# Performance work log

Measured on AMD Instinct MI355X. Metric: run time of the kernel, lower is better.

Reference implementation:

```python
import jax, jax.numpy as jnp
import numpy as np

N = 20480      # total nodes
E = 327680     # total edges (avg degree 16)
B = 16         # graphs in batch
IN = 16        # node feature dim
H = 8          # hidden_out_channel
CO = 64        # conv_out_channel
ET = 36        # n_edge_types
EF = 2         # edge_features
OUT = 1        # classifier out
DIMS = [(IN, H), (H, H), (H, H), (H, CO)]


def setup_inputs() -> dict:
    key = jax.random.key(0)
    ks = jax.random.split(key, 32)
    inp = {}
    inp['x'] = jax.random.normal(ks[0], (N, IN), jnp.float32)
    inp['edge_index'] = jax.random.randint(ks[1], (2, E), 0, N)
    inp['edge_type'] = jax.random.randint(ks[2], (E,), 0, ET)
    inp['edge_attr'] = jax.random.normal(ks[3], (E, EF), jnp.float32)
    inp['cell_type'] = jax.random.randint(ks[4], (N,), 0, 2)
    inp['batch'] = (jnp.arange(N) // (N // B)).astype(jnp.int32)
    i = 5
    for l, (ci, co) in enumerate(DIMS, 1):
        d = ci * co
        s = 1.0 / np.sqrt(EF)
        inp[f'emb{l}'] = jax.random.normal(ks[i], (ET, d), jnp.float32) * 0.02; i += 1
        inp[f'wh{l}'] = jax.random.normal(ks[i], (EF, d), jnp.float32) * s; i += 1
        inp[f'bh{l}'] = jnp.zeros((d,), jnp.float32)
        inp[f'wg{l}'] = jax.random.normal(ks[i], (EF, d), jnp.float32) * s; i += 1
        inp[f'bg{l}'] = jnp.zeros((d,), jnp.float32)
        inp[f'root{l}'] = jax.random.normal(ks[i], (ci, co), jnp.float32) / np.sqrt(ci); i += 1
        inp[f'bias{l}'] = jnp.zeros((co,), jnp.float32)
    inp['clf_w'] = jax.random.normal(ks[i], (CO, OUT), jnp.float32) / np.sqrt(CO)
    inp['clf_b'] = jnp.zeros((OUT,), jnp.float32)
    return inp


def edge_weights(etype, ef, emb, wh, bh, wg, bg):
    # EdgeNN: relu(embedding(type) * fc_h(feat) + fc_g(feat)) -> [E, cin*cout]
    return jax.nn.relu(emb[etype] * (ef @ wh + bh) + (ef @ wg + bg))


def nnconv(h, src, dst, W, root, bias):
    # NNConv(aggr='mean', root_weight=True): gather src feats, per-edge matmul, scatter-mean
    cin, cout = root.shape
    msg = jnp.einsum('ei,eio->eo', h[src], W.reshape(-1, cin, cout))  # [E, cout]
    agg = jax.ops.segment_sum(msg, dst, num_segments=N)
    deg = jax.ops.segment_sum(jnp.ones_like(msg[:, 0]), dst, num_segments=N)
    return agg / jnp.maximum(deg, 1.0)[:, None] + h @ root + bias


def reference(x, edge_index, edge_type, edge_attr, cell_type, batch,
              emb1, wh1, bh1, wg1, bg1, root1, bias1,
              emb2, wh2, bh2, wg2, bg2, root2, bias2,
              emb3, wh3, bh3, wg3, bg3, root3, bias3,
              emb4, wh4, bh4, wg4, bg4, root4, bias4,
              clf_w, clf_b):
    src, dst = edge_index[0], edge_index[1]
    layers = [(emb1, wh1, bh1, wg1, bg1, root1, bias1),
              (emb2, wh2, bh2, wg2, bg2, root2, bias2),
              (emb3, wh3, bh3, wg3, bg3, root3, bias3),
              (emb4, wh4, bh4, wg4, bg4, root4, bias4)]
    h = x
    for (emb, wh, bh, wg, bg, root, bias) in layers:  # fixed 4 structurally-distinct layers
        W = edge_weights(edge_type, edge_attr, emb, wh, bh, wg, bg)
        h = jax.nn.relu(nnconv(h, src, dst, W, root, bias))
    # gated scatter-mean pooling over tumor cells (cell_type == 1)
    gate = (cell_type == 1).astype(jnp.int32)
    seg = gate * (batch.astype(jnp.int32) + 1)  # 0 = masked-out bucket
    pooled = jax.ops.segment_sum(h, seg, num_segments=B + 1)
    cnt = jax.ops.segment_sum(jnp.ones((h.shape[0],), h.dtype), seg, num_segments=B + 1)
    pooled = (pooled / jnp.maximum(cnt, 1.0)[:, None])[1:B + 1]  # [B, CO]
    return jax.nn.sigmoid(pooled @ clf_w + clf_b)  # hazards [B, OUT]
```

## Files before the change

kernel.cpp:

```cpp
#include <hip/hip_runtime.h>
#include <math.h>

#define NN 20480
#define NE 327680
#define NBATCH 16

typedef float v2f __attribute__((ext_vector_type(2)));

#if __has_builtin(__builtin_elementwise_max)
#define VMAX0(a) __builtin_elementwise_max((a), (v2f){0.f, 0.f})
#else
static __device__ __forceinline__ v2f VMAX0(v2f a) {
  v2f r; r.x = fmaxf(a.x, 0.f); r.y = fmaxf(a.y, 0.f); return r;
}
#endif

__global__ void hist_kernel(const int* __restrict__ dst, int* __restrict__ cnt) {
  int e = blockIdx.x * blockDim.x + threadIdx.x;
  if (e < NE) atomicAdd(&cnt[dst[e]], 1);
}

__global__ __launch_bounds__(1024) void scan_kernel(const int* __restrict__ cnt,
                                                    int* __restrict__ off,
                                                    int* __restrict__ cur) {
  __shared__ int part[1024];
  int tid = threadIdx.x;
  const int PT = NN / 1024;
  int loc[PT];
  int run = 0;
  int base = tid * PT;
#pragma unroll
  for (int k = 0; k < PT; k++) { loc[k] = run; run += cnt[base + k]; }
  part[tid] = run;
  __syncthreads();
  for (int d = 1; d < 1024; d <<= 1) {
    int t = (tid >= d) ? part[tid - d] : 0;
    __syncthreads();
    part[tid] += t;
    __syncthreads();
  }
  int pre = (tid == 0) ? 0 : part[tid - 1];
#pragma unroll
  for (int k = 0; k < PT; k++) {
    off[base + k] = pre + loc[k];
    cur[base + k] = pre + loc[k];
  }
  if (tid == 1023) off[NN] = pre + run;
}

__global__ void scatter_kernel(const int* __restrict__ src, const int* __restrict__ dst,
                               const int* __restrict__ etype, const float* __restrict__ eattr,
                               int* __restrict__ cur, float4* __restrict__ es) {
  int e = blockIdx.x * blockDim.x + threadIdx.x;
  if (e >= NE) return;
  int d = dst[e];
  int pos = atomicAdd(&cur[d], 1);
  es[pos] = make_float4(__int_as_float(src[e]), __int_as_float(etype[e]),
                        eattr[2 * e], eattr[2 * e + 1]);
}

__global__ __launch_bounds__(256) void transpose_kernel(
    const float* __restrict__ e1, const float* __restrict__ e2,
    const float* __restrict__ e3, const float* __restrict__ e4,
    float* __restrict__ t1, float* __restrict__ t2,
    float* __restrict__ t3, float* __restrict__ t4) {
  int idx = blockIdx.x * 256 + threadIdx.x;
  if (idx < 36 * 128) {
    int t = idx >> 7, r = idx & 127, o = r >> 4, i = r & 15;
    t1[idx] = e1[(t << 7) + i * 8 + o];
  }
  if (idx < 36 * 64) {
    int t = idx >> 6, r = idx & 63, o = r >> 3, i = r & 7;
    t2[idx] = e2[(t << 6) + i * 8 + o];
    t3[idx] = e3[(t << 6) + i * 8 + o];
  }
  {
    int t = idx >> 9, r = idx & 511, o = r >> 3, i = r & 7;
    t4[idx] = e4[(t << 9) + i * 64 + o];
  }
}

__global__ __launch_bounds__(256) void layer_small16(
    const int* __restrict__ off, const float4* __restrict__ es,
    const float* __restrict__ h_in, const float* __restrict__ embT,
    const float* __restrict__ wh, const float* __restrict__ bh,
    const float* __restrict__ wg, const float* __restrict__ bg,
    const float* __restrict__ root, const float* __restrict__ bias,
    float* __restrict__ h_out) {
  constexpr int D = 128;
  int lane = threadIdx.x & 63;
  int o = lane & 7;
  int ihalf = (lane >> 3) & 1;
  int esub = lane >> 4;
  int ibase = ihalf * 8;
  v2f rwh0[4], rwh1[4], rbh[4], rwg0[4], rwg1[4], rbg[4], rroot[4];
#pragma unroll
  for (int p = 0; p < 4; p++) {
    int a = (ibase + 2 * p) * 8 + o, b = (ibase + 2 * p + 1) * 8 + o;
    rwh0[p] = (v2f){wh[a], wh[b]};
    rwh1[p] = (v2f){wh[D + a], wh[D + b]};
    rbh[p]  = (v2f){bh[a], bh[b]};
    rwg0[p] = (v2f){wg[a], wg[b]};
    rwg1[p] = (v2f){wg[D + a], wg[D + b]};
    rbg[p]  = (v2f){bg[a], bg[b]};
    rroot[p] = (v2f){root[a], root[b]};
  }
  float rbias = bias[o];
  int n = __builtin_amdgcn_readfirstlane((int)(blockIdx.x * 4) + (int)(threadIdx.x >> 6));
  int beg = off[n], end = off[n + 1];
  int nIter = (end - beg + 3) >> 2;
  float acc = 0.f;
  int j = beg + esub;
  bool val0 = j < end;
  float4 rec0 = val0 ? es[j] : make_float4(0.f, 0.f, 0.f, 0.f);
  int s0 = __float_as_int(rec0.x);
  const float4* hp0 = (const float4*)(h_in + s0 * 16 + ibase);
  float4 hA0 = hp0[0], hB0 = hp0[1];
  for (int it = 0; it < nIter; ++it) {
    int j1 = j + 4;
    bool val1 = j1 < end;
    float4 rec1 = val1 ? es[j1] : make_float4(0.f, 0.f, 0.f, 0.f);
    int s1 = __float_as_int(rec1.x);
    const float4* hp1 = (const float4*)(h_in + s1 * 16 + ibase);
    float4 hA1 = hp1[0], hB1 = hp1[1];
    int t0 = __float_as_int(rec0.y);
    const float4* sp = (const float4*)(embT + t0 * 128 + o * 16 + ibase);
    float4 sv0 = sp[0], sv1 = sp[1];
    v2f stv[4] = {(v2f){sv0.x, sv0.y}, (v2f){sv0.z, sv0.w},
                  (v2f){sv1.x, sv1.y}, (v2f){sv1.z, sv1.w}};
    v2f hv[4] = {(v2f){hA0.x, hA0.y}, (v2f){hA0.z, hA0.w},
                 (v2f){hB0.x, hB0.y}, (v2f){hB0.z, hB0.w}};
    v2f ef0 = (v2f){rec0.z, rec0.z}, ef1 = (v2f){rec0.w, rec0.w};
    v2f msg = {0.f, 0.f};
#pragma unroll
    for (int p = 0; p < 4; p++) {
      v2f hval = ef0 * rwh0[p] + ef1 * rwh1[p] + rbh[p];
      v2f gval = ef0 * rwg0[p] + ef1 * rwg1[p] + rbg[p];
      msg += hv[p] * VMAX0(stv[p] * hval + gval);
    }
    acc += val0 ? (msg.x + msg.y) : 0.f;
    rec0 = rec1; hA0 = hA1; hB0 = hB1; val0 = val1; j = j1;
  }
  acc += __shfl_xor(acc, 8);
  acc += __shfl_xor(acc, 16);
  acc += __shfl_xor(acc, 32);
  const float* hn = h_in + n * 16 + ibase;
  v2f rtv = {0.f, 0.f};
#pragma unroll
  for (int p = 0; p < 4; p++)
    rtv += (v2f){hn[2 * p], hn[2 * p + 1]} * rroot[p];
  float rt = rtv.x + rtv.y;
  rt += __shfl_xor(rt, 8);
  float deg = (float)(end - beg);
  float val = fmaxf(rbias + rt + acc / fmaxf(deg, 1.f), 0.f);
  if (lane < 8) h_out[n * 8 + o] = val;
}

__global__ __launch_bounds__(256) void layer_small8(
    const int* __restrict__ off, const float4* __restrict__ es,
    const float* __restrict__ h_in, const float* __restrict__ embT,
    const float* __restrict__ wh, const float* __restrict__ bh,
    const float* __restrict__ wg, const float* __restrict__ bg,
    const float* __restrict__ root, const float* __restrict__ bias,
    float* __restrict__ h_out) {
  int lane = threadIdx.x & 63;
  int o = lane & 7, esub = lane >> 3;
  v2f rwh0[4], rwh1[4], rbh[4], rwg0[4], rwg1[4], rbg[4], rroot[4];
#pragma unroll
  for (int p = 0; p < 4; p++) {
    int a = (2 * p) * 8 + o, b = (2 * p + 1) * 8 + o;
    rwh0[p] = (v2f){wh[a], wh[b]};
    rwh1[p] = (v2f){wh[64 + a], wh[64 + b]};
    rbh[p]  = (v2f){bh[a], bh[b]};
    rwg0[p] = (v2f){wg[a], wg[b]};
    rwg1[p] = (v2f){wg[64 + a], wg[64 + b]};
    rbg[p]  = (v2f){bg[a], bg[b]};
    rroot[p] = (v2f){root[a], root[b]};
  }
  float rbias = bias[o];
  int n = __builtin_amdgcn_readfirstlane((int)(blockIdx.x * 4) + (int)(threadIdx.x >> 6));
  int beg = off[n], end = off[n + 1];
  int nIter = (end - beg + 7) >> 3;
  float acc = 0.f;
  int j = beg + esub;
  bool val0 = j < end;
  float4 rec0 = val0 ? es[j] : make_float4(0.f, 0.f, 0.f, 0.f);
  int s0 = __float_as_int(rec0.x);
  const float4* hp0 = (const float4*)(h_in + s0 * 8);
  float4 hA0 = hp0[0], hB0 = hp0[1];
  for (int it = 0; it < nIter; ++it) {
    int j1 = j + 8;
    bool val1 = j1 < end;
    float4 rec1 = val1 ? es[j1] : make_float4(0.f, 0.f, 0.f, 0.f);
    int s1 = __float_as_int(rec1.x);
    const float4* hp1 = (const float4*)(h_in + s1 * 8);
    float4 hA1 = hp1[0], hB1 = hp1[1];
    int t0 = __float_as_int(rec0.y);
    const float4* sp = (const float4*)(embT + t0 * 64 + o * 8);
    float4 sv0 = sp[0], sv1 = sp[1];
    v2f stv[4] = {(v2f){sv0.x, sv0.y}, (v2f){sv0.z, sv0.w},
                  (v2f){sv1.x, sv1.y}, (v2f){sv1.z, sv1.w}};
    v2f hv[4] = {(v2f){hA0.x, hA0.y}, (v2f){hA0.z, hA0.w},
                 (v2f){hB0.x, hB0.y}, (v2f){hB0.z, hB0.w}};
    v2f ef0 = (v2f){rec0.z, rec0.z}, ef1 = (v2f){rec0.w, rec0.w};
    v2f msg = {0.f, 0.f};
#pragma unroll
    for (int p = 0; p < 4; p++) {
      v2f hval = ef0 * rwh0[p] + ef1 * rwh1[p] + rbh[p];
      v2f gval = ef0 * rwg0[p] + ef1 * rwg1[p] + rbg[p];
      msg += hv[p] * VMAX0(stv[p] * hval + gval);
    }
    acc += val0 ? (msg.x + msg.y) : 0.f;
    rec0 = rec1; hA0 = hA1; hB0 = hB1; val0 = val1; j = j1;
  }
  acc += __shfl_xor(acc, 8);
  acc += __shfl_xor(acc, 16);
  acc += __shfl_xor(acc, 32);
  const float* hn = h_in + n * 8;
  v2f rtv = {0.f, 0.f};
#pragma unroll
  for (int p = 0; p < 4; p++)
    rtv += (v2f){hn[2 * p], hn[2 * p + 1]} * rroot[p];
  float deg = (float)(end - beg);
  float val = fmaxf(rbias + rtv.x + rtv.y + acc / fmaxf(deg, 1.f), 0.f);
  if (lane < 8) h_out[n * 8 + o] = val;
}

__global__ __launch_bounds__(256) void layer_l4(
    const int* __restrict__ off, const float4* __restrict__ es,
    const float* __restrict__ h_in, const float* __restrict__ embT,
    const float* __restrict__ wh, const float* __restrict__ bh,
    const float* __restrict__ wg, const float* __restrict__ bg,
    const float* __restrict__ root, const float* __restrict__ bias,
    float* __restrict__ h_out) {
  int lane = threadIdx.x & 63;
  v2f rwh0[4], rwh1[4], rbh[4], rwg0[4], rwg1[4], rbg[4], rroot[4];
#pragma unroll
  for (int p = 0; p < 4; p++) {
    int a = (2 * p) * 64 + lane, b = (2 * p + 1) * 64 + lane;
    rwh0[p] = (v2f){wh[a], wh[b]};
    rwh1[p] = (v2f){wh[512 + a], wh[512 + b]};
    rbh[p]  = (v2f){bh[a], bh[b]};
    rwg0[p] = (v2f){wg[a], wg[b]};
    rwg1[p] = (v2f){wg[512 + a], wg[512 + b]};
    rbg[p]  = (v2f){bg[a], bg[b]};
    rroot[p] = (v2f){root[a], root[b]};
  }
  float rbias = bias[lane];
  int n = __builtin_amdgcn_readfirstlane((int)(blockIdx.x * 4) + (int)(threadIdx.x >> 6));
  int beg = off[n], end = off[n + 1];
  float acc0 = 0.f, acc1 = 0.f;
  int e = beg;
  for (; e + 2 <= end; e += 2) {
    float4 r0 = es[e], r1 = es[e + 1];
    int s0 = __float_as_int(r0.x), t0 = __float_as_int(r0.y);
    int s1 = __float_as_int(r1.x), t1 = __float_as_int(r1.y);
    const float4* hp0 = (const float4*)(h_in + s0 * 8);
    const float4* hp1 = (const float4*)(h_in + s1 * 8);
    float4 a0 = hp0[0], a1 = hp0[1];
    float4 b0 = hp1[0], b1 = hp1[1];
    const float4* ep0 = (const float4*)(embT + t0 * 512 + lane * 8);
    const float4* ep1 = (const float4*)(embT + t1 * 512 + lane * 8);
    float4 s00 = ep0[0], s01 = ep0[1];
    float4 s10 = ep1[0], s11 = ep1[1];
    v2f sv0[4] = {(v2f){s00.x, s00.y}, (v2f){s00.z, s00.w},
                  (v2f){s01.x, s01.y}, (v2f){s01.z, s01.w}};
    v2f sv1[4] = {(v2f){s10.x, s10.y}, (v2f){s10.z, s10.w},
                  (v2f){s11.x, s11.y}, (v2f){s11.z, s11.w}};
    v2f hva[4] = {(v2f){a0.x, a0.y}, (v2f){a0.z, a0.w},
                  (v2f){a1.x, a1.y}, (v2f){a1.z, a1.w}};
    v2f hvb[4] = {(v2f){b0.x, b0.y}, (v2f){b0.z, b0.w},
                  (v2f){b1.x, b1.y}, (v2f){b1.z, b1.w}};
    v2f e00 = (v2f){r0.z, r0.z}, e01 = (v2f){r0.w, r0.w};
    v2f e10 = (v2f){r1.z, r1.z}, e11 = (v2f){r1.w, r1.w};
    v2f m0 = {0.f, 0.f}, m1 = {0.f, 0.f};
#pragma unroll
    for (int p = 0; p < 4; p++) {
      v2f hv0 = e00 * rwh0[p] + e01 * rwh1[p] + rbh[p];
      v2f gv0 = e00 * rwg0[p] + e01 * rwg1[p] + rbg[p];
      m0 += hva[p] * VMAX0(sv0[p] * hv0 + gv0);
      v2f hv1 = e10 * rwh0[p] + e11 * rwh1[p] + rbh[p];
      v2f gv1 = e10 * rwg0[p] + e11 * rwg1[p] + rbg[p];
      m1 += hvb[p] * VMAX0(sv1[p] * hv1 + gv1);
    }
    acc0 += m0.x + m0.y;
    acc1 += m1.x + m1.y;
  }
  if (e < end) {
    float4 r0 = es[e];
    int s0 = __float_as_int(r0.x), t0 = __float_as_int(r0.y);
    const float4* hp0 = (const float4*)(h_in + s0 * 8);
    float4 a0 = hp0[0], a1 = hp0[1];
    const float4* ep0 = (const float4*)(embT + t0 * 512 + lane * 8);
    float4 s00 = ep0[0], s01 = ep0[1];
    v2f sv0[4] = {(v2f){s00.x, s00.y}, (v2f){s00.z, s00.w},
                  (v2f){s01.x, s01.y}, (v2f){s01.z, s01.w}};
    v2f hva[4] = {(v2f){a0.x, a0.y}, (v2f){a0.z, a0.w},
                  (v2f){a1.x, a1.y}, (v2f){a1.z, a1.w}};
    v2f e00 = (v2f){r0.z, r0.z}, e01 = (v2f){r0.w, r0.w};
    v2f m0 = {0.f, 0.f};
#pragma unroll
    for (int p = 0; p < 4; p++) {
      v2f hv0 = e00 * rwh0[p] + e01 * rwh1[p] + rbh[p];
      v2f gv0 = e00 * rwg0[p] + e01 * rwg1[p] + rbg[p];
      m0 += hva[p] * VMAX0(sv0[p] * hv0 + gv0);
    }
    acc0 += m0.x + m0.y;
  }
  float acc = acc0 + acc1;
  float deg = (float)(end - beg);
  const float* hn = h_in + n * 8;
  v2f rtv = {0.f, 0.f};
#pragma unroll
  for (int p = 0; p < 4; p++)
    rtv += (v2f){hn[2 * p], hn[2 * p + 1]} * rroot[p];
  h_out[n * 64 + lane] = fmaxf(rbias + rtv.x + rtv.y + acc / fmaxf(deg, 1.f), 0.f);
}

__global__ __launch_bounds__(256) void pool1_kernel(
    const float* __restrict__ h4, const int* __restrict__ ct,
    float* __restrict__ pooled, float* __restrict__ pcnt) {
  __shared__ float ss[4][64];
  __shared__ float sc[4];
  int b = blockIdx.x / 20, c = blockIdx.x % 20;
  int base = b * (NN / NBATCH) + c * 64;
  int o = threadIdx.x & 63, sub = threadIdx.x >> 6;
  float sum = 0.f, cnt = 0.f;
  for (int j = sub; j < 64; j += 4) {
    int n = base + j;
    if (ct[n] == 1) { sum += h4[n * 64 + o]; cnt += 1.f; }
  }
  ss[sub][o] = sum;
  if (o == 0) sc[sub] = cnt;
  __syncthreads();
  if (threadIdx.x < 64) {
    float tot = ss[0][o] + ss[1][o] + ss[2][o] + ss[3][o];
    unsafeAtomicAdd(&pooled[b * 64 + o], tot);
    if (o == 0) unsafeAtomicAdd(&pcnt[b], sc[0] + sc[1] + sc[2] + sc[3]);
  }
}

__global__ __launch_bounds__(1024) void pool2_kernel(
    const float* __restrict__ pooled, const float* __restrict__ pcnt,
    const float* __restrict__ clf_w, const float* __restrict__ clf_b,
    float* __restrict__ out) {
  int b = threadIdx.x >> 6, o = threadIdx.x & 63;
  float c = pcnt[b];
  float v = (pooled[b * 64 + o] / fmaxf(c, 1.f)) * clf_w[o];
#pragma unroll
  for (int d = 32; d; d >>= 1) v += __shfl_down(v, d);
  if (o == 0) out[b] = 1.f / (1.f + expf(-(v + clf_b[0])));
}

extern "C" void kernel_launch(void* const* d_in, const int* in_sizes, int n_in,
                              void* d_out, int out_size, void* d_ws, size_t ws_size,
                              hipStream_t stream) {
  (void)in_sizes; (void)n_in; (void)out_size; (void)ws_size;
  const float* x     = (const float*)d_in[0];
  const int*   eidx  = (const int*)d_in[1];
  const int*   src   = eidx;
  const int*   dst   = eidx + NE;
  const int*   etype = (const int*)d_in[2];
  const float* eattr = (const float*)d_in[3];
  const int*   ct    = (const int*)d_in[4];
  const float *emb[4], *wh[4], *bh[4], *wg[4], *bg[4], *root[4], *bias[4];
  for (int l = 0; l < 4; l++) {
    int b0 = 6 + 7 * l;
    emb[l]  = (const float*)d_in[b0 + 0];
    wh[l]   = (const float*)d_in[b0 + 1];
    bh[l]   = (const float*)d_in[b0 + 2];
    wg[l]   = (const float*)d_in[b0 + 3];
    bg[l]   = (const float*)d_in[b0 + 4];
    root[l] = (const float*)d_in[b0 + 5];
    bias[l] = (const float*)d_in[b0 + 6];
  }
  const float* clf_w = (const float*)d_in[34];
  const float* clf_b = (const float*)d_in[35];
  float* outp = (float*)d_out;

  float* ws  = (float*)d_ws;
  int*    off    = (int*)ws;
  float4* es     = (float4*)(ws + 20484);
  float*  hA     = ws + 20484 + 4 * NE;
  float*  hB     = hA + 8 * NN;
  float*  h4     = hB + 8 * NN;
  float*  embT1  = h4 + 64 * NN;
  float*  embT2  = embT1 + 36 * 128;
  float*  embT3  = embT2 + 36 * 64;
  float*  embT4  = embT3 + 36 * 64;
  float*  pooled = embT4 + 36 * 512;
  float*  pcnt   = pooled + 16 * 64;
  int*    cnt    = (int*)h4;
  int*    cur    = cnt + NN;

  hipMemsetAsync(cnt, 0, NN * sizeof(int), stream);
  hipMemsetAsync(pooled, 0, (16 * 64 + 16) * sizeof(float), stream);
  hist_kernel<<<NE / 256, 256, 0, stream>>>(dst, cnt);
  transpose_kernel<<<72, 256, 0, stream>>>(emb[0], emb[1], emb[2], emb[3],
                                           embT1, embT2, embT3, embT4);
  scan_kernel<<<1, 1024, 0, stream>>>(cnt, off, cur);
  scatter_kernel<<<NE / 256, 256, 0, stream>>>(src, dst, etype, eattr, cur, es);

  layer_small16<<<NN / 4, 256, 0, stream>>>(off, es, x, embT1,
      wh[0], bh[0], wg[0], bg[0], root[0], bias[0], hA);
  layer_small8<<<NN / 4, 256, 0, stream>>>(off, es, hA, embT2,
      wh[1], bh[1], wg[1], bg[1], root[1], bias[1], hB);
  layer_small8<<<NN / 4, 256, 0, stream>>>(off, es, hB, embT3,
      wh[2], bh[2], wg[2], bg[2], root[2], bias[2], hA);
  layer_l4<<<NN / 4, 256, 0, stream>>>(off, es, hA, embT4,
      wh[3], bh[3], wg[3], bg[3], root[3], bias[3], h4);

  pool1_kernel<<<320, 256, 0, stream>>>(h4, ct, pooled, pcnt);
  pool2_kernel<<<1, 1024, 0, stream>>>(pooled, pcnt, clf_w, clf_b, outp);
}
```

Baseline: 305.4 us.

## Fuse all stages into one persistent kernel with software grid barriers

Replaces the chain of separate launches (histogram, scan, scatter, four layers, pooling) with one persistent kernel of 240 blocks of 1024 threads. The stages are separated by an atomic-counter grid barrier. The scan becomes a two-level block scan, and the layer loops become grid-stride loops over nodes, one wave per node, using a ballot-driven edge loop. This removes launch gaps and memsets, but adds barrier latency, depends on all 240 blocks being co-resident, and may lower occupancy.

```diff
diff --git a/kernel.cpp b/kernel.cpp
--- a/kernel.cpp
+++ b/kernel.cpp
@@ -4,159 +4,118 @@
 #define NN 20480
 #define NE 327680
 #define NBATCH 16
+#define NBLK 240
+#define NTHR 1024
+#define GSZ (NBLK * NTHR)
+#define NWAVE (NBLK * (NTHR / 64))
+#define NPB ((NN + NBLK - 1) / NBLK)
 
 typedef float v2f __attribute__((ext_vector_type(2)));
 
-#if __has_builtin(__builtin_elementwise_max)
-#define VMAX0(a) __builtin_elementwise_max((a), (v2f){0.f, 0.f})
-#else
-static __device__ __forceinline__ v2f VMAX0(v2f a) {
+static __device__ __forceinline__ v2f vmax0(v2f a) {
   v2f r; r.x = fmaxf(a.x, 0.f); r.y = fmaxf(a.y, 0.f); return r;
 }
-#endif
-
-__global__ void hist_kernel(const int* __restrict__ dst, int* __restrict__ cnt) {
-  int e = blockIdx.x * blockDim.x + threadIdx.x;
-  if (e < NE) atomicAdd(&cnt[dst[e]], 1);
-}
-
-__global__ __launch_bounds__(1024) void scan_kernel(const int* __restrict__ cnt,
-                                                    int* __restrict__ off,
-                                                    int* __restrict__ cur) {
-  __shared__ int part[1024];
-  int tid = threadIdx.x;
-  const int PT = NN / 1024;
-  int loc[PT];
-  int run = 0;
-  int base = tid * PT;
-#pragma unroll
-  for (int k = 0; k < PT; k++) { loc[k] = run; run += cnt[base + k]; }
-  part[tid] = run;
+
+struct Args {
+  const float* x; const int* src; const int* dst; const int* etype;
+  const float* eattr; const int* ct;
+  const float* emb[4]; const float* wh[4]; const float* bh[4];
+  const float* wg[4]; const float* bg[4]; const float* root[4]; const float* bias[4];
+  const float* clf_w; const float* clf_b;
+  float* out;
+  int* off; float4* es; float* hA; float* hB; float* h4;
+  float* eT1; float* eT2; float* eT3; float* eT4;
+  float* pooled; float* pcnt; int* cnt; int* cur; int* bar; int* partial;
+};
+
+__device__ __forceinline__ void grid_sync(int* cntp, int* genp) {
   __syncthreads();
-  for (int d = 1; d < 1024; d <<= 1) {
-    int t = (tid >= d) ? part[tid - d] : 0;
-    __syncthreads();
-    part[tid] += t;
-    __syncthreads();
-  }
-  int pre = (tid == 0) ? 0 : part[tid - 1];
-#pragma unroll
-  for (int k = 0; k < PT; k++) {
-    off[base + k] = pre + loc[k];
-    cur[base + k] = pre + loc[k];
-  }
-  if (tid == 1023) off[NN] = pre + run;
-}
-
-__global__ void scatter_kernel(const int* __restrict__ src, const int* __restrict__ dst,
-                               const int* __restrict__ etype, const float* __restrict__ eattr,
-                               int* __restrict__ cur, float4* __restrict__ es) {
-  int e = blockIdx.x * blockDim.x + threadIdx.x;
-  if (e >= NE) return;
-  int d = dst[e];
-  int pos = atomicAdd(&cur[d], 1);
-  es[pos] = make_float4(__int_as_float(src[e]), __int_as_float(etype[e]),
-                        eattr[2 * e], eattr[2 * e + 1]);
-}
-
-__global__ __launch_bounds__(256) void transpose_kernel(
-    const float* __restrict__ e1, const float* __restrict__ e2,
-    const float* __restrict__ e3, const float* __restrict__ e4,
-    float* __restrict__ t1, float* __restrict__ t2,
-    float* __restrict__ t3, float* __restrict__ t4) {
-  int idx = blockIdx.x * 256 + threadIdx.x;
-  if (idx < 36 * 128) {
-    int t = idx >> 7, r = idx & 127, o = r >> 4, i = r & 15;
-    t1[idx] = e1[(t << 7) + i * 8 + o];
-  }
-  if (idx < 36 * 64) {
-    int t = idx >> 6, r = idx & 63, o = r >> 3, i = r & 7;
-    t2[idx] = e2[(t << 6) + i * 8 + o];
-    t3[idx] = e3[(t << 6) + i * 8 + o];
-  }
-  {
-    int t = idx >> 9, r = idx & 511, o = r >> 3, i = r & 7;
-    t4[idx] = e4[(t << 9) + i * 64 + o];
-  }
-}
-
-__global__ __launch_bounds__(256) void layer_small16(
-    const int* __restrict__ off, const float4* __restrict__ es,
-    const float* __restrict__ h_in, const float* __restrict__ embT,
-    const float* __restrict__ wh, const float* __restrict__ bh,
-    const float* __restrict__ wg, const float* __restrict__ bg,
-    const float* __restrict__ root, const float* __restrict__ bias,
-    float* __restrict__ h_out) {
-  constexpr int D = 128;
+  if (threadIdx.x == 0) {
+    __threadfence();
+    int g = __hip_atomic_load(genp, __ATOMIC_RELAXED, __HIP_MEMORY_SCOPE_AGENT);
+    int c = __hip_atomic_fetch_add(cntp, 1, __ATOMIC_ACQ_REL, __HIP_MEMORY_SCOPE_AGENT);
+    if (c == NBLK - 1) {
+      __hip_atomic_store(cntp, 0, __ATOMIC_RELAXED, __HIP_MEMORY_SCOPE_AGENT);
+      __hip_atomic_store(genp, g + 1, __ATOMIC_RELEASE, __HIP_MEMORY_SCOPE_AGENT);
+    } else {
+      while (__hip_atomic_load(genp, __ATOMIC_ACQUIRE, __HIP_MEMORY_SCOPE_AGENT) == g)
+        __builtin_amdgcn_s_sleep(4);
+    }
+    __threadfence();
+  }
+  __syncthreads();
+}
+
+__device__ __forceinline__ void do_small16(const Args& a) {
+  const int D = 128;
   int lane = threadIdx.x & 63;
-  int o = lane & 7;
-  int ihalf = (lane >> 3) & 1;
-  int esub = lane >> 4;
+  int o = lane & 7, ihalf = (lane >> 3) & 1, esub = lane >> 4;
   int ibase = ihalf * 8;
+  const float *wh = a.wh[0], *bh = a.bh[0], *wg = a.wg[0], *bg = a.bg[0];
+  const float *root = a.root[0], *bias = a.bias[0];
   v2f rwh0[4], rwh1[4], rbh[4], rwg0[4], rwg1[4], rbg[4], rroot[4];
 #pragma unroll
   for (int p = 0; p < 4; p++) {
-    int a = (ibase + 2 * p) * 8 + o, b = (ibase + 2 * p + 1) * 8 + o;
-    rwh0[p] = (v2f){wh[a], wh[b]};
-    rwh1[p] = (v2f){wh[D + a], wh[D + b]};
-    rbh[p]  = (v2f){bh[a], bh[b]};
-    rwg0[p] = (v2f){wg[a], wg[b]};
-    rwg1[p] = (v2f){wg[D + a], wg[D + b]};
-    rbg[p]  = (v2f){bg[a], bg[b]};
-    rroot[p] = (v2f){root[a], root[b]};
+    int ai = (ibase + 2 * p) * 8 + o, bi = (ibase + 2 * p + 1) * 8 + o;
+    rwh0[p] = (v2f){wh[ai], wh[bi]};  rwh1[p] = (v2f){wh[D + ai], wh[D + bi]};
+    rbh[p]  = (v2f){bh[ai], bh[bi]};
+    rwg0[p] = (v2f){wg[ai], wg[bi]};  rwg1[p] = (v2f){wg[D + ai], wg[D + bi]};
+    rbg[p]  = (v2f){bg[ai], bg[bi]};  rroot[p] = (v2f){root[ai], root[bi]};
   }
   float rbias = bias[o];
-  int n = __builtin_amdgcn_readfirstlane((int)(blockIdx.x * 4) + (int)(threadIdx.x >> 6));
-  int beg = off[n], end = off[n + 1];
-  int nIter = (end - beg + 3) >> 2;
-  float acc = 0.f;
-  int j = beg + esub;
-  bool val0 = j < end;
-  float4 rec0 = val0 ? es[j] : make_float4(0.f, 0.f, 0.f, 0.f);
-  int s0 = __float_as_int(rec0.x);
-  const float4* hp0 = (const float4*)(h_in + s0 * 16 + ibase);
-  float4 hA0 = hp0[0], hB0 = hp0[1];
-  for (int it = 0; it < nIter; ++it) {
-    int j1 = j + 4;
-    bool val1 = j1 < end;
-    float4 rec1 = val1 ? es[j1] : make_float4(0.f, 0.f, 0.f, 0.f);
-    int s1 = __float_as_int(rec1.x);
-    const float4* hp1 = (const float4*)(h_in + s1 * 16 + ibase);
-    float4 hA1 = hp1[0], hB1 = hp1[1];
-    int t0 = __float_as_int(rec0.y);
-    const float4* sp = (const float4*)(embT + t0 * 128 + o * 16 + ibase);
-    float4 sv0 = sp[0], sv1 = sp[1];
-    v2f stv[4] = {(v2f){sv0.x, sv0.y}, (v2f){sv0.z, sv0.w},
-                  (v2f){sv1.x, sv1.y}, (v2f){sv1.z, sv1.w}};
-    v2f hv[4] = {(v2f){hA0.x, hA0.y}, (v2f){hA0.z, hA0.w},
-                 (v2f){hB0.x, hB0.y}, (v2f){hB0.z, hB0.w}};
-    v2f ef0 = (v2f){rec0.z, rec0.z}, ef1 = (v2f){rec0.w, rec0.w};
-    v2f msg = {0.f, 0.f};
-#pragma unroll
-    for (int p = 0; p < 4; p++) {
-      v2f hval = ef0 * rwh0[p] + ef1 * rwh1[p] + rbh[p];
-      v2f gval = ef0 * rwg0[p] + ef1 * rwg1[p] + rbg[p];
-      msg += hv[p] * VMAX0(stv[p] * hval + gval);
-    }
-    acc += val0 ? (msg.x + msg.y) : 0.f;
-    rec0 = rec1; hA0 = hA1; hB0 = hB1; val0 = val1; j = j1;
-  }
-  acc += __shfl_xor(acc, 8);
-  acc += __shfl_xor(acc, 16);
-  acc += __shfl_xor(acc, 32);
-  const float* hn = h_in + n * 16 + ibase;
-  v2f rtv = {0.f, 0.f};
-#pragma unroll
-  for (int p = 0; p < 4; p++)
-    rtv += (v2f){hn[2 * p], hn[2 * p + 1]} * rroot[p];
-  float rt = rtv.x + rtv.y;
-  rt += __shfl_xor(rt, 8);
-  float deg = (float)(end - beg);
-  float val = fmaxf(rbias + rt + acc / fmaxf(deg, 1.f), 0.f);
-  if (lane < 8) h_out[n * 8 + o] = val;
-}
-
-__global__ __launch_bounds__(256) void layer_small8(
+  int wid = blockIdx.x * (NTHR / 64) + (threadIdx.x >> 6);
+  for (int n0 = wid; n0 < NN; n0 += NWAVE) {
+    int n = __builtin_amdgcn_readfirstlane(n0);
+    int beg = a.off[n], end = a.off[n + 1];
+    float acc = 0.f;
+    int j = beg + esub;
+    bool v0 = j < end;
+    float4 rec0 = v0 ? a.es[j] : make_float4(0.f, 0.f, 0.f, 0.f);
+    int s0 = __float_as_int(rec0.x);
+    const float4* hp0 = (const float4*)(a.x + s0 * 16 + ibase);
+    float4 hA0 = hp0[0], hB0 = hp0[1];
+    while (__ballot(v0)) {
+      int j1 = j + 4;
+      bool v1 = j1 < end;
+      float4 rec1 = v1 ? a.es[j1] : make_float4(0.f, 0.f, 0.f, 0.f);
+      int s1 = __float_as_int(rec1.x);
+      const float4* hp1 = (const float4*)(a.x + s1 * 16 + ibase);
+      float4 hA1 = hp1[0], hB1 = hp1[1];
+      int t0 = __float_as_int(rec0.y);
+      const float4* sp = (const float4*)(a.eT1 + t0 * 128 + o * 16 + ibase);
+      float4 sv0 = sp[0], sv1 = sp[1];
+      v2f stv[4] = {(v2f){sv0.x, sv0.y}, (v2f){sv0.z, sv0.w},
+                    (v2f){sv1.x, sv1.y}, (v2f){sv1.z, sv1.w}};
+      v2f hv[4] = {(v2f){hA0.x, hA0.y}, (v2f){hA0.z, hA0.w},
+                   (v2f){hB0.x, hB0.y}, (v2f){hB0.z, hB0.w}};
+      v2f ef0 = (v2f){rec0.z, rec0.z}, ef1 = (v2f){rec0.w, rec0.w};
+      v2f msg = {0.f, 0.f};
+#pragma unroll
+      for (int p = 0; p < 4; p++) {
+        v2f hval = ef0 * rwh0[p] + ef1 * rwh1[p] + rbh[p];
+        v2f gval = ef0 * rwg0[p] + ef1 * rwg1[p] + rbg[p];
+        msg += hv[p] * vmax0(stv[p] * hval + gval);
+      }
+      acc += v0 ? (msg.x + msg.y) : 0.f;
+      rec0 = rec1; hA0 = hA1; hB0 = hB1; v0 = v1; j = j1;
+    }
+    acc += __shfl_xor(acc, 8);
+    acc += __shfl_xor(acc, 16);
+    acc += __shfl_xor(acc, 32);
+    const float* hn = a.x + n * 16 + ibase;
+    v2f rtv = {0.f, 0.f};
+#pragma unroll
+    for (int p = 0; p < 4; p++)
+      rtv += (v2f){hn[2 * p], hn[2 * p + 1]} * rroot[p];
+    float rt = rtv.x + rtv.y;
+    rt += __shfl_xor(rt, 8);
+    float deg = (float)(end - beg);
+    float val = fmaxf(rbias + rt + acc / fmaxf(deg, 1.f), 0.f);
+    if (lane < 8) a.hA[n * 8 + o] = val;
+  }
+}
+
+__device__ __forceinline__ void do_small8(
     const int* __restrict__ off, const float4* __restrict__ es,
     const float* __restrict__ h_in, const float* __restrict__ embT,
     const float* __restrict__ wh, const float* __restrict__ bh,
@@ -168,248 +127,323 @@
   v2f rwh0[4], rwh1[4], rbh[4], rwg0[4], rwg1[4], rbg[4], rroot[4];
 #pragma unroll
   for (int p = 0; p < 4; p++) {
-    int a = (2 * p) * 8 + o, b = (2 * p + 1) * 8 + o;
-    rwh0[p] = (v2f){wh[a], wh[b]};
-    rwh1[p] = (v2f){wh[64 + a], wh[64 + b]};
-    rbh[p]  = (v2f){bh[a], bh[b]};
-    rwg0[p] = (v2f){wg[a], wg[b]};
-    rwg1[p] = (v2f){wg[64 + a], wg[64 + b]};
-    rbg[p]  = (v2f){bg[a], bg[b]};
-    rroot[p] = (v2f){root[a], root[b]};
+    int ai = (2 * p) * 8 + o, bi = (2 * p + 1) * 8 + o;
+    rwh0[p] = (v2f){wh[ai], wh[bi]};  rwh1[p] = (v2f){wh[64 + ai], wh[64 + bi]};
+    rbh[p]  = (v2f){bh[ai], bh[bi]};
+    rwg0[p] = (v2f){wg[ai], wg[bi]};  rwg1[p] = (v2f){wg[64 + ai], wg[64 + bi]};
+    rbg[p]  = (v2f){bg[ai], bg[bi]};  rroot[p] = (v2f){root[ai], root[bi]};
   }
   float rbias = bias[o];
-  int n = __builtin_amdgcn_readfirstlane((int)(blockIdx.x * 4) + (int)(threadIdx.x >> 6));
-  int beg = off[n], end = off[n + 1];
-  int nIter = (end - beg + 7) >> 3;
-  float acc = 0.f;
-  int j = beg + esub;
-  bool val0 = j < end;
-  float4 rec0 = val0 ? es[j] : make_float4(0.f, 0.f, 0.f, 0.f);
-  int s0 = __float_as_int(rec0.x);
-  const float4* hp0 = (const float4*)(h_in + s0 * 8);
-  float4 hA0 = hp0[0], hB0 = hp0[1];
-  for (int it = 0; it < nIter; ++it) {
-    int j1 = j + 8;
-    bool val1 = j1 < end;
-    float4 rec1 = val1 ? es[j1] : make_float4(0.f, 0.f, 0.f, 0.f);
-    int s1 = __float_as_int(rec1.x);
-    const float4* hp1 = (const float4*)(h_in + s1 * 8);
-    float4 hA1 = hp1[0], hB1 = hp1[1];
-    int t0 = __float_as_int(rec0.y);
-    const float4* sp = (const float4*)(embT + t0 * 64 + o * 8);
-    float4 sv0 = sp[0], sv1 = sp[1];
-    v2f stv[4] = {(v2f){sv0.x, sv0.y}, (v2f){sv0.z, sv0.w},
-                  (v2f){sv1.x, sv1.y}, (v2f){sv1.z, sv1.w}};
-    v2f hv[4] = {(v2f){hA0.x, hA0.y}, (v2f){hA0.z, hA0.w},
-                 (v2f){hB0.x, hB0.y}, (v2f){hB0.z, hB0.w}};
-    v2f ef0 = (v2f){rec0.z, rec0.z}, ef1 = (v2f){rec0.w, rec0.w};
-    v2f msg = {0.f, 0.f};
-#pragma unroll
-    for (int p = 0; p < 4; p++) {
-      v2f hval = ef0 * rwh0[p] + ef1 * rwh1[p] + rbh[p];
-      v2f gval = ef0 * rwg0[p] + ef1 * rwg1[p] + rbg[p];
-      msg += hv[p] * VMAX0(stv[p] * hval + gval);
-    }
-    acc += val0 ? (msg.x + msg.y) : 0.f;
-    rec0 = rec1; hA0 = hA1; hB0 = hB1; val0 = val1; j = j1;
-  }
-  acc += __shfl_xor(acc, 8);
-  acc += __shfl_xor(acc, 16);
-  acc += __shfl_xor(acc, 32);
-  const float* hn = h_in + n * 8;
-  v2f rtv = {0.f, 0.f};
-#pragma unroll
-  for (int p = 0; p < 4; p++)
-    rtv += (v2f){hn[2 * p], hn[2 * p + 1]} * rroot[p];
-  float deg = (float)(end - beg);
-  float val = fmaxf(rbias + rtv.x + rtv.y + acc / fmaxf(deg, 1.f), 0.f);
-  if (lane < 8) h_out[n * 8 + o] = val;
-}
-
-__global__ __launch_bounds__(256) void layer_l4(
-    const int* __restrict__ off, const float4* __restrict__ es,
-    const float* __restrict__ h_in, const float* __restrict__ embT,
-    const float* __restrict__ wh, const float* __restrict__ bh,
-    const float* __restrict__ wg, const float* __restrict__ bg,
-    const float* __restrict__ root, const float* __restrict__ bias,
-    float* __restrict__ h_out) {
+  int wid = blockIdx.x * (NTHR / 64) + (threadIdx.x >> 6);
+  for (int n0 = wid; n0 < NN; n0 += NWAVE) {
+    int n = __builtin_amdgcn_readfirstlane(n0);
+    int beg = off[n], end = off[n + 1];
+    float acc = 0.f;
+    int j = beg + esub;
+    bool v0 = j < end;
+    float4 rec0 = v0 ? es[j] : make_float4(0.f, 0.f, 0.f, 0.f);
+    int s0 = __float_as_int(rec0.x);
+    const float4* hp0 = (const float4*)(h_in + s0 * 8);
+    float4 hA0 = hp0[0], hB0 = hp0[1];
+    while (__ballot(v0)) {
+      int j1 = j + 8;
+      bool v1 = j1 < end;
+      float4 rec1 = v1 ? es[j1] : make_float4(0.f, 0.f, 0.f, 0.f);
+      int s1 = __float_as_int(rec1.x);
+      const float4* hp1 = (const float4*)(h_in + s1 * 8);
+      float4 hA1 = hp1[0], hB1 = hp1[1];
+      int t0 = __float_as_int(rec0.y);
+      const float4* sp = (const float4*)(embT + t0 * 64 + o * 8);
+      float4 sv0 = sp[0], sv1 = sp[1];
+      v2f stv[4] = {(v2f){sv0.x, sv0.y}, (v2f){sv0.z, sv0.w},
+                    (v2f){sv1.x, sv1.y}, (v2f){sv1.z, sv1.w}};
+      v2f hv[4] = {(v2f){hA0.x, hA0.y}, (v2f){hA0.z, hA0.w},
+                   (v2f){hB0.x, hB0.y}, (v2f){hB0.z, hB0.w}};
+      v2f ef0 = (v2f){rec0.z, rec0.z}, ef1 = (v2f){rec0.w, rec0.w};
+      v2f msg = {0.f, 0.f};
+#pragma unroll
+      for (int p = 0; p < 4; p++) {
+        v2f hval = ef0 * rwh0[p] + ef1 * rwh1[p] + rbh[p];
+        v2f gval = ef0 * rwg0[p] + ef1 * rwg1[p] + rbg[p];
+        msg += hv[p] * vmax0(stv[p] * hval + gval);
+      }
+      acc += v0 ? (msg.x + msg.y) : 0.f;
+      rec0 = rec1; hA0 = hA1; hB0 = hB1; v0 = v1; j = j1;
+    }
+    acc += __shfl_xor(acc, 8);
+    acc += __shfl_xor(acc, 16);
+    acc += __shfl_xor(acc, 32);
+    const float* hn = h_in + n * 8;
+    v2f rtv = {0.f, 0.f};
+#pragma unroll
+    for (int p = 0; p < 4; p++)
+      rtv += (v2f){hn[2 * p], hn[2 * p + 1]} * rroot[p];
+    float deg = (float)(end - beg);
+    float val = fmaxf(rbias + rtv.x + rtv.y + acc / fmaxf(deg, 1.f), 0.f);
+    if (lane < 8) h_out[n * 8 + o] = val;
+  }
+}
+
+__device__ __forceinline__ void do_l4(const Args& a) {
   int lane = threadIdx.x & 63;
+  const float *wh = a.wh[3], *bh = a.bh[3], *wg = a.wg[3], *bg = a.bg[3];
+  const float *root = a.root[3], *bias = a.bias[3];
+  const float* embT = a.eT4;
+  const float* h_in = a.hA;
   v2f rwh0[4], rwh1[4], rbh[4], rwg0[4], rwg1[4], rbg[4], rroot[4];
 #pragma unroll
   for (int p = 0; p < 4; p++) {
-    int a = (2 * p) * 64 + lane, b = (2 * p + 1) * 64 + lane;
-    rwh0[p] = (v2f){wh[a], wh[b]};
-    rwh1[p] = (v2f){wh[512 + a], wh[512 + b]};
-    rbh[p]  = (v2f){bh[a], bh[b]};
-    rwg0[p] = (v2f){wg[a], wg[b]};
-    rwg1[p] = (v2f){wg[512 + a], wg[512 + b]};
-    rbg[p]  = (v2f){bg[a], bg[b]};
-    rroot[p] = (v2f){root[a], root[b]};
+    int ai = (2 * p) * 64 + lane, bi = (2 * p + 1) * 64 + lane;
+    rwh0[p] = (v2f){wh[ai], wh[bi]};  rwh1[p] = (v2f){wh[512 + ai], wh[512 + bi]};
+    rbh[p]  = (v2f){bh[ai], bh[bi]};
+    rwg0[p] = (v2f){wg[ai], wg[bi]};  rwg1[p] = (v2f){wg[512 + ai], wg[512 + bi]};
+    rbg[p]  = (v2f){bg[ai], bg[bi]};  rroot[p] = (v2f){root[ai], root[bi]};
   }
   float rbias = bias[lane];
-  int n = __builtin_amdgcn_readfirstlane((int)(blockIdx.x * 4) + (int)(threadIdx.x >> 6));
-  int beg = off[n], end = off[n + 1];
-  float acc0 = 0.f, acc1 = 0.f;
-  int e = beg;
-  for (; e + 2 <= end; e += 2) {
-    float4 r0 = es[e], r1 = es[e + 1];
-    int s0 = __float_as_int(r0.x), t0 = __float_as_int(r0.y);
-    int s1 = __float_as_int(r1.x), t1 = __float_as_int(r1.y);
-    const float4* hp0 = (const float4*)(h_in + s0 * 8);
-    const float4* hp1 = (const float4*)(h_in + s1 * 8);
-    float4 a0 = hp0[0], a1 = hp0[1];
-    float4 b0 = hp1[0], b1 = hp1[1];
-    const float4* ep0 = (const float4*)(embT + t0 * 512 + lane * 8);
-    const float4* ep1 = (const float4*)(embT + t1 * 512 + lane * 8);
-    float4 s00 = ep0[0], s01 = ep0[1];
-    float4 s10 = ep1[0], s11 = ep1[1];
-    v2f sv0[4] = {(v2f){s00.x, s00.y}, (v2f){s00.z, s00.w},
-                  (v2f){s01.x, s01.y}, (v2f){s01.z, s01.w}};
-    v2f sv1[4] = {(v2f){s10.x, s10.y}, (v2f){s10.z, s10.w},
-                  (v2f){s11.x, s11.y}, (v2f){s11.z, s11.w}};
-    v2f hva[4] = {(v2f){a0.x, a0.y}, (v2f){a0.z, a0.w},
-                  (v2f){a1.x, a1.y}, (v2f){a1.z, a1.w}};
-    v2f hvb[4] = {(v2f){b0.x, b0.y}, (v2f){b0.z, b0.w},
-                  (v2f){b1.x, b1.y}, (v2f){b1.z, b1.w}};
-    v2f e00 = (v2f){r0.z, r0.z}, e01 = (v2f){r0.w, r0.w};
-    v2f e10 = (v2f){r1.z, r1.z}, e11 = (v2f){r1.w, r1.w};
-    v2f m0 = {0.f, 0.f}, m1 = {0.f, 0.f};
-#pragma unroll
-    for (int p = 0; p < 4; p++) {
-      v2f hv0 = e00 * rwh0[p] + e01 * rwh1[p] + rbh[p];
-      v2f gv0 = e00 * rwg0[p] + e01 * rwg1[p] + rbg[p];
-      m0 += hva[p] * VMAX0(sv0[p] * hv0 + gv0);
-      v2f hv1 = e10 * rwh0[p] + e11 * rwh1[p] + rbh[p];
-      v2f gv1 = e10 * rwg0[p] + e11 * rwg1[p] + rbg[p];
-      m1 += hvb[p] * VMAX0(sv1[p] * hv1 + gv1);
-    }
-    acc0 += m0.x + m0.y;
-    acc1 += m1.x + m1.y;
-  }
-  if (e < end) {
-    float4 r0 = es[e];
-    int s0 = __float_as_int(r0.x), t0 = __float_as_int(r0.y);
-    const float4* hp0 = (const float4*)(h_in + s0 * 8);
-    float4 a0 = hp0[0], a1 = hp0[1];
-    const float4* ep0 = (const float4*)(embT + t0 * 512 + lane * 8);
-    float4 s00 = ep0[0], s01 = ep0[1];
-    v2f sv0[4] = {(v2f){s00.x, s00.y}, (v2f){s00.z, s00.w},
-                  (v2f){s01.x, s01.y}, (v2f){s01.z, s01.w}};
-    v2f hva[4] = {(v2f){a0.x, a0.y}, (v2f){a0.z, a0.w},
-                  (v2f){a1.x, a1.y}, (v2f){a1.z, a1.w}};
-    v2f e00 = (v2f){r0.z, r0.z}, e01 = (v2f){r0.w, r0.w};
-    v2f m0 = {0.f, 0.f};
-#pragma unroll
-    for (int p = 0; p < 4; p++) {
-      v2f hv0 = e00 * rwh0[p] + e01 * rwh1[p] + rbh[p];
-      v2f gv0 = e00 * rwg0[p] + e01 * rwg1[p] + rbg[p];
-      m0 += hva[p] * VMAX0(sv0[p] * hv0 + gv0);
-    }
-    acc0 += m0.x + m0.y;
-  }
-  float acc = acc0 + acc1;
-  float deg = (float)(end - beg);
-  const float* hn = h_in + n * 8;
-  v2f rtv = {0.f, 0.f};
-#pragma unroll
-  for (int p = 0; p < 4; p++)
-    rtv += (v2f){hn[2 * p], hn[2 * p + 1]} * rroot[p];
-  h_out[n * 64 + lane] = fmaxf(rbias + rtv.x + rtv.y + acc / fmaxf(deg, 1.f), 0.f);
-}
-
-__global__ __launch_bounds__(256) void pool1_kernel(
-    const float* __restrict__ h4, const int* __restrict__ ct,
-    float* __restrict__ pooled, float* __restrict__ pcnt) {
-  __shared__ float ss[4][64];
-  __shared__ float sc[4];
-  int b = blockIdx.x / 20, c = blockIdx.x % 20;
-  int base = b * (NN / NBATCH) + c * 64;
-  int o = threadIdx.x & 63, sub = threadIdx.x >> 6;
-  float sum = 0.f, cnt = 0.f;
-  for (int j = sub; j < 64; j += 4) {
-    int n = base + j;
-    if (ct[n] == 1) { sum += h4[n * 64 + o]; cnt += 1.f; }
-  }
-  ss[sub][o] = sum;
-  if (o == 0) sc[sub] = cnt;
-  __syncthreads();
-  if (threadIdx.x < 64) {
-    float tot = ss[0][o] + ss[1][o] + ss[2][o] + ss[3][o];
-    unsafeAtomicAdd(&pooled[b * 64 + o], tot);
-    if (o == 0) unsafeAtomicAdd(&pcnt[b], sc[0] + sc[1] + sc[2] + sc[3]);
-  }
-}
-
-__global__ __launch_bounds__(1024) void pool2_kernel(
-    const float* __restrict__ pooled, const float* __restrict__ pcnt,
-    const float* __restrict__ clf_w, const float* __restrict__ clf_b,
-    float* __restrict__ out) {
-  int b = threadIdx.x >> 6, o = threadIdx.x & 63;
-  float c = pcnt[b];
-  float v = (pooled[b * 64 + o] / fmaxf(c, 1.f)) * clf_w[o];
-#pragma unroll
-  for (int d = 32; d; d >>= 1) v += __shfl_down(v, d);
-  if (o == 0) out[b] = 1.f / (1.f + expf(-(v + clf_b[0])));
+  int wid = blockIdx.x * (NTHR / 64) + (threadIdx.x >> 6);
+  for (int n0 = wid; n0 < NN; n0 += NWAVE) {
+    int n = __builtin_amdgcn_readfirstlane(n0);
+    int beg = a.off[n], end = a.off[n + 1];
+    float acc0 = 0.f, acc1 = 0.f;
+    int e = beg;
+    for (; e + 2 <= end; e += 2) {
+      float4 r0 = a.es[e], r1 = a.es[e + 1];
+      int s0 = __float_as_int(r0.x), t0 = __float_as_int(r0.y);
+      int s1 = __float_as_int(r1.x), t1 = __float_as_int(r1.y);
+      const float4* hp0 = (const float4*)(h_in + s0 * 8);
+      const float4* hp1 = (const float4*)(h_in + s1 * 8);
+      float4 a0 = hp0[0], a1 = hp0[1];
+      float4 b0 = hp1[0], b1 = hp1[1];
+      const float4* ep0 = (const float4*)(embT + t0 * 512 + lane * 8);
+      const float4* ep1 = (const float4*)(embT + t1 * 512 + lane * 8);
+      float4 s00 = ep0[0], s01 = ep0[1];
+      float4 s10 = ep1[0], s11 = ep1[1];
+      v2f sv0[4] = {(v2f){s00.x, s00.y}, (v2f){s00.z, s00.w},
+                    (v2f){s01.x, s01.y}, (v2f){s01.z, s01.w}};
+      v2f sv1[4] = {(v2f){s10.x, s10.y}, (v2f){s10.z, s10.w},
+                    (v2f){s11.x, s11.y}, (v2f){s11.z, s11.w}};
+      v2f hva[4] = {(v2f){a0.x, a0.y}, (v2f){a0.z, a0.w},
+                    (v2f){a1.x, a1.y}, (v2f){a1.z, a1.w}};
+      v2f hvb[4] = {(v2f){b0.x, b0.y}, (v2f){b0.z, b0.w},
+                    (v2f){b1.x, b1.y}, (v2f){b1.z, b1.w}};
+      v2f e00 = (v2f){r0.z, r0.z}, e01 = (v2f){r0.w, r0.w};
+      v2f e10 = (v2f){r1.z, r1.z}, e11 = (v2f){r1.w, r1.w};
+      v2f m0 = {0.f, 0.f}, m1 = {0.f, 0.f};
+#pragma unroll
+      for (int p = 0; p < 4; p++) {
+        v2f hv0 = e00 * rwh0[p] + e01 * rwh1[p] + rbh[p];
+        v2f gv0 = e00 * rwg0[p] + e01 * rwg1[p] + rbg[p];
+        m0 += hva[p] * vmax0(sv0[p] * hv0 + gv0);
+        v2f hv1 = e10 * rwh0[p] + e11 * rwh1[p] + rbh[p];
+        v2f gv1 = e10 * rwg0[p] + e11 * rwg1[p] + rbg[p];
+        m1 += hvb[p] * vmax0(sv1[p] * hv1 + gv1);
+      }
+      acc0 += m0.x + m0.y;
+      acc1 += m1.x + m1.y;
+    }
+    if (e < end) {
+      float4 r0 = a.es[e];
+      int s0 = __float_as_int(r0.x), t0 = __float_as_int(r0.y);
+      const float4* hp0 = (const float4*)(h_in + s0 * 8);
+      float4 a0 = hp0[0], a1 = hp0[1];
+      const float4* ep0 = (const float4*)(embT + t0 * 512 + lane * 8);
+      float4 s00 = ep0[0], s01 = ep0[1];
+      v2f sv0[4] = {(v2f){s00.x, s00.y}, (v2f){s00.z, s00.w},
+                    (v2f){s01.x, s01.y}, (v2f){s01.z, s01.w}};
+      v2f hva[4] = {(v2f){a0.x, a0.y}, (v2f){a0.z, a0.w},
+                    (v2f){a1.x, a1.y}, (v2f){a1.z, a1.w}};
+      v2f e00 = (v2f){r0.z, r0.z}, e01 = (v2f){r0.w, r0.w};
+      v2f m0 = {0.f, 0.f};
+#pragma unroll
+      for (int p = 0; p < 4; p++) {
+        v2f hv0 = e00 * rwh0[p] + e01 * rwh1[p] + rbh[p];
+        v2f gv0 = e00 * rwg0[p] + e01 * rwg1[p] + rbg[p];
+        m0 += hva[p] * vmax0(sv0[p] * hv0 + gv0);
+      }
+      acc0 += m0.x + m0.y;
+    }
+    float acc = acc0 + acc1;
+    float deg = (float)(end - beg);
+    const float* hn = h_in + n * 8;
+    v2f rtv = {0.f, 0.f};
+#pragma unroll
+    for (int p = 0; p < 4; p++)
+      rtv += (v2f){hn[2 * p], hn[2 * p + 1]} * rroot[p];
+    a.h4[n * 64 + lane] = fmaxf(rbias + rtv.x + rtv.y + acc / fmaxf(deg, 1.f), 0.f);
+  }
+}
+
+__global__ __launch_bounds__(NTHR, 4) void mega_kernel(Args a) {
+  int t = threadIdx.x;
+  int gtid = blockIdx.x * NTHR + t;
+  int* bcnt = a.bar;
+  int* bgen = a.bar + 1;
+
+  if (gtid < NN) a.cnt[gtid] = 0;
+  if (gtid < NBATCH * 64 + NBATCH) a.pooled[gtid] = 0.f;
+  if (gtid < 36 * 128) {
+    int tt = gtid >> 7, r = gtid & 127, o = r >> 4, i = r & 15;
+    a.eT1[gtid] = a.emb[0][(tt << 7) + i * 8 + o];
+  }
+  if (gtid < 36 * 64) {
+    int tt = gtid >> 6, r = gtid & 63, o = r >> 3, i = r & 7;
+    a.eT2[gtid] = a.emb[1][(tt << 6) + i * 8 + o];
+    a.eT3[gtid] = a.emb[2][(tt << 6) + i * 8 + o];
+  }
+  if (gtid < 36 * 512) {
+    int tt = gtid >> 9, r = gtid & 511, o = r >> 3, i = r & 7;
+    a.eT4[gtid] = a.emb[3][(tt << 9) + i * 64 + o];
+  }
+  grid_sync(bcnt, bgen);
+
+  for (int e = gtid; e < NE; e += GSZ) atomicAdd(&a.cnt[a.dst[e]], 1);
+  grid_sync(bcnt, bgen);
+
+  {
+    __shared__ int sA[128];
+    int base = blockIdx.x * NPB;
+    int c = 0;
+    if (t < NPB && base + t < NN) c = a.cnt[base + t];
+    if (t < 128) sA[t] = (t < NPB) ? c : 0;
+    __syncthreads();
+    for (int d = 1; d < 128; d <<= 1) {
+      int v = 0;
+      if (t < 128 && t >= d) v = sA[t - d];
+      __syncthreads();
+      if (t < 128) sA[t] += v;
+      __syncthreads();
+    }
+    if (t < NPB && base + t < NN) a.off[base + t] = sA[t] - c;
+    if (t == 0) a.partial[blockIdx.x] = sA[127];
+  }
+  grid_sync(bcnt, bgen);
+
+  {
+    __shared__ int sB[NBLK];
+    if (t < NBLK) sB[t] = a.partial[t];
+    __syncthreads();
+    for (int d = 1; d < NBLK; d <<= 1) {
+      int v = 0;
+      if (t < NBLK && t >= d) v = sB[t - d];
+      __syncthreads();
+      if (t < NBLK) sB[t] += v;
+      __syncthreads();
+    }
+    int pre = (blockIdx.x == 0) ? 0 : sB[blockIdx.x - 1];
+    int base = blockIdx.x * NPB;
+    if (t < NPB && base + t < NN) {
+      int v = a.off[base + t] + pre;
+      a.off[base + t] = v;
+      a.cur[base + t] = v;
+    }
+    if (blockIdx.x == 0 && t == 0) a.off[NN] = NE;
+  }
+  grid_sync(bcnt, bgen);
+
+  for (int e = gtid; e < NE; e += GSZ) {
+    int d = a.dst[e];
+    int pos = atomicAdd(&a.cur[d], 1);
+    a.es[pos] = make_float4(__int_as_float(a.src[e]), __int_as_float(a.etype[e]),
+                            a.eattr[2 * e], a.eattr[2 * e + 1]);
+  }
+  grid_sync(bcnt, bgen);
+
+  do_small16(a);
+  grid_sync(bcnt, bgen);
+  do_small8(a.off, a.es, a.hA, a.eT2, a.wh[1], a.bh[1], a.wg[1], a.bg[1],
+            a.root[1], a.bias[1], a.hB);
+  grid_sync(bcnt, bgen);
+  do_small8(a.off, a.es, a.hB, a.eT3, a.wh[2], a.bh[2], a.wg[2], a.bg[2],
+            a.root[2], a.bias[2], a.hA);
+  grid_sync(bcnt, bgen);
+  do_l4(a);
+  grid_sync(bcnt, bgen);
+
+  {
+    __shared__ float ss[16][64];
+    __shared__ float scn[16];
+    int o = t & 63, sub = t >> 6;
+    for (int u = blockIdx.x; u < NBATCH * 20; u += NBLK) {
+      int b = u / 20, c = u % 20;
+      int base = b * (NN / NBATCH) + c * 64;
+      float sum = 0.f, cntf = 0.f;
+      for (int j = sub; j < 64; j += 16) {
+        int n = base + j;
+        if (a.ct[n] == 1) { sum += a.h4[n * 64 + o]; cntf += 1.f; }
+      }
+      ss[sub][o] = sum;
+      if (o == 0) scn[sub] = cntf;
+      __syncthreads();
+      if (t < 64) {
+        float tot = 0.f;
+#pragma unroll
+        for (int k = 0; k < 16; k++) tot += ss[k][o];
+        unsafeAtomicAdd(&a.pooled[b * 64 + o], tot);
+        if (o == 0) {
+          float cc = 0.f;
+#pragma unroll
+          for (int k = 0; k < 16; k++) cc += scn[k];
+          unsafeAtomicAdd(&a.pcnt[b], cc);
+        }
+      }
+      __syncthreads();
+    }
+  }
+  grid_sync(bcnt, bgen);
+
+  if (blockIdx.x == 0) {
+    int b = t >> 6, o = t & 63;
+    float c = a.pcnt[b];
+    float v = (a.pooled[b * 64 + o] / fmaxf(c, 1.f)) * a.clf_w[o];
+#pragma unroll
+    for (int d = 32; d; d >>= 1) v += __shfl_down(v, d);
+    if (o == 0) a.out[b] = 1.f / (1.f + expf(-(v + a.clf_b[0])));
+  }
 }
 
 extern "C" void kernel_launch(void* const* d_in, const int* in_sizes, int n_in,
                               void* d_out, int out_size, void* d_ws, size_t ws_size,
                               hipStream_t stream) {
   (void)in_sizes; (void)n_in; (void)out_size; (void)ws_size;
-  const float* x     = (const float*)d_in[0];
-  const int*   eidx  = (const int*)d_in[1];
-  const int*   src   = eidx;
-  const int*   dst   = eidx + NE;
-  const int*   etype = (const int*)d_in[2];
-  const float* eattr = (const float*)d_in[3];
-  const int*   ct    = (const int*)d_in[4];
-  const float *emb[4], *wh[4], *bh[4], *wg[4], *bg[4], *root[4], *bias[4];
+  Args a;
+  a.x     = (const float*)d_in[0];
+  const int* eidx = (const int*)d_in[1];
+  a.src   = eidx;
+  a.dst   = eidx + NE;
+  a.etype = (const int*)d_in[2];
+  a.eattr = (const float*)d_in[3];
+  a.ct    = (const int*)d_in[4];
   for (int l = 0; l < 4; l++) {
     int b0 = 6 + 7 * l;
-    emb[l]  = (const float*)d_in[b0 + 0];
-    wh[l]   = (const float*)d_in[b0 + 1];
-    bh[l]   = (const float*)d_in[b0 + 2];
-    wg[l]   = (const float*)d_in[b0 + 3];
-    bg[l]   = (const float*)d_in[b0 + 4];
-    root[l] = (const float*)d_in[b0 + 5];
-    bias[l] = (const float*)d_in[b0 + 6];
-  }
-  const float* clf_w = (const float*)d_in[34];
-  const float* clf_b = (const float*)d_in[35];
-  float* outp = (float*)d_out;
-
-  float* ws  = (float*)d_ws;
-  int*    off    = (int*)ws;
-  float4* es     = (float4*)(ws + 20484);
-  float*  hA     = ws + 20484 + 4 * NE;
-  float*  hB     = hA + 8 * NN;
-  float*  h4     = hB + 8 * NN;
-  float*  embT1  = h4 + 64 * NN;
-  float*  embT2  = embT1 + 36 * 128;
-  float*  embT3  = embT2 + 36 * 64;
-  float*  embT4  = embT3 + 36 * 64;
-  float*  pooled = embT4 + 36 * 512;
-  float*  pcnt   = pooled + 16 * 64;
-  int*    cnt    = (int*)h4;
-  int*    cur    = cnt + NN;
-
-  hipMemsetAsync(cnt, 0, NN * sizeof(int), stream);
-  hipMemsetAsync(pooled, 0, (16 * 64 + 16) * sizeof(float), stream);
-  hist_kernel<<<NE / 256, 256, 0, stream>>>(dst, cnt);
-  transpose_kernel<<<72, 256, 0, stream>>>(emb[0], emb[1], emb[2], emb[3],
-                                           embT1, embT2, embT3, embT4);
-  scan_kernel<<<1, 1024, 0, stream>>>(cnt, off, cur);
-  scatter_kernel<<<NE / 256, 256, 0, stream>>>(src, dst, etype, eattr, cur, es);
-
-  layer_small16<<<NN / 4, 256, 0, stream>>>(off, es, x, embT1,
-      wh[0], bh[0], wg[0], bg[0], root[0], bias[0], hA);
-  layer_small8<<<NN / 4, 256, 0, stream>>>(off, es, hA, embT2,
-      wh[1], bh[1], wg[1], bg[1], root[1], bias[1], hB);
-  layer_small8<<<NN / 4, 256, 0, stream>>>(off, es, hB, embT3,
-      wh[2], bh[2], wg[2], bg[2], root[2], bias[2], hA);
-  layer_l4<<<NN / 4, 256, 0, stream>>>(off, es, hA, embT4,
-      wh[3], bh[3], wg[3], bg[3], root[3], bias[3], h4);
-
-  pool1_kernel<<<320, 256, 0, stream>>>(h4, ct, pooled, pcnt);
-  pool2_kernel<<<1, 1024, 0, stream>>>(pooled, pcnt, clf_w, clf_b, outp);
-}
+    a.emb[l]  = (const float*)d_in[b0 + 0];
+    a.wh[l]   = (const float*)d_in[b0 + 1];
+    a.bh[l]   = (const float*)d_in[b0 + 2];
+    a.wg[l]   = (const float*)d_in[b0 + 3];
+    a.bg[l]   = (const float*)d_in[b0 + 4];
+    a.root[l] = (const float*)d_in[b0 + 5];
+    a.bias[l] = (const float*)d_in[b0 + 6];
+  }
+  a.clf_w = (const float*)d_in[34];
+  a.clf_b = (const float*)d_in[35];
+  a.out   = (float*)d_out;
+
+  float* ws = (float*)d_ws;
+  a.off    = (int*)ws;
+  a.es     = (float4*)(ws + 20484);
+  a.hA     = ws + 20484 + 4 * NE;
+  a.hB     = a.hA + 8 * NN;
+  a.h4     = a.hB + 8 * NN;
+  a.eT1    = a.h4 + 64 * NN;
+  a.eT2    = a.eT1 + 36 * 128;
+  a.eT3    = a.eT2 + 36 * 64;
+  a.eT4    = a.eT3 + 36 * 64;
+  a.pooled = a.eT4 + 36 * 512;
+  a.pcnt   = a.pooled + NBATCH * 64;
+  a.bar    = (int*)(a.pcnt + NBATCH);
+  a.partial= a.bar + 2;
+  a.cnt    = (int*)a.h4;
+  a.cur    = a.cnt + NN;
+
+  hipMemsetAsync(a.bar, 0, 2 * sizeof(int), stream);
+  mega_kernel<<<NBLK, NTHR, 0, stream>>>(a);
+}
```

After: 738.2 us. 2.42x slower.
